# Optimization experiments

Hardware: AMD Instinct MI355X
Metric: run time of the kernel (lower is better)

## Reference

```python
import jax, jax.numpy as jnp
import numpy as np

T, B, E, H, P, D = 500, 1024, 26, 100, 80, 64  # frames, batch, embed, hidden, phonemes, dict_size


def gru_layer(xs, h0, Wih, Whh, bih, bhh):
    """PyTorch-convention GRU over time-major xs [T,B,in]; h0 [B,H]."""
    def step(h, x):
        gi = x @ Wih.T + bih          # [B,3H]
        gh = h @ Whh.T + bhh          # [B,3H]
        i_r, i_z, i_n = jnp.split(gi, 3, axis=-1)
        h_r, h_z, h_n = jnp.split(gh, 3, axis=-1)
        r = jax.nn.sigmoid(i_r + h_r)
        z = jax.nn.sigmoid(i_z + h_z)
        n = jnp.tanh(i_n + r * h_n)
        h_new = (1.0 - z) * n + z * h
        return h_new, h_new
    h_last, ys = jax.lax.scan(step, h0, xs)
    return ys, h_last


def _p(k, shape):
    return jax.random.normal(k, shape, dtype=jnp.float32) * 0.1


def setup_inputs() -> dict:
    key = jax.random.key(0)
    ks = jax.random.split(key, 20)
    inp = {
        "x": jax.random.normal(ks[0], (T, B, E), dtype=jnp.float32),
        "target": jax.random.randint(ks[1], (P, B, 1), 0, D).astype(jnp.int64),
        "emb": _p(ks[2], (D, E)),
        # encoder 2-layer GRU
        "enc_Wih0": _p(ks[3], (3 * H, E)), "enc_Whh0": _p(ks[4], (3 * H, H)),
        "enc_bih0": _p(ks[5], (3 * H,)),  "enc_bhh0": _p(ks[6], (3 * H,)),
        "enc_Wih1": _p(ks[7], (3 * H, H)), "enc_Whh1": _p(ks[8], (3 * H, H)),
        "enc_bih1": _p(ks[9], (3 * H,)),  "enc_bhh1": _p(ks[10], (3 * H,)),
        # decoder 2-layer GRU
        "dec_Wih0": _p(ks[11], (3 * H, E)), "dec_Whh0": _p(ks[12], (3 * H, H)),
        "dec_bih0": _p(ks[13], (3 * H,)),  "dec_bhh0": _p(ks[14], (3 * H,)),
        "dec_Wih1": _p(ks[15], (3 * H, H)), "dec_Whh1": _p(ks[16], (3 * H, H)),
        "dec_bih1": _p(ks[17], (3 * H,)),  "dec_bhh1": _p(ks[18], (3 * H,)),
        "lin_W": _p(ks[19], (D, H)),
        "lin_b": jnp.zeros((D,), dtype=jnp.float32),
    }
    return inp


def reference(x, target, emb,
              enc_Wih0, enc_Whh0, enc_bih0, enc_bhh0,
              enc_Wih1, enc_Whh1, enc_bih1, enc_bhh1,
              dec_Wih0, dec_Whh0, dec_bih0, dec_bhh0,
              dec_Wih1, dec_Whh1, dec_bih1, dec_bhh1,
              lin_W, lin_b):
    batch = x.shape[1]
    h0 = jnp.zeros((batch, H), dtype=x.dtype)
    # Encoder (dropout in eval mode = identity)
    e0, h_enc0 = gru_layer(x, h0, enc_Wih0, enc_Whh0, enc_bih0, enc_bhh0)
    e1, h_enc1 = gru_layer(e0, h0, enc_Wih1, enc_Whh1, enc_bih1, enc_bhh1)
    # Decoder with full teacher forcing: inputs are target[0..P-1]
    dec_in = emb[target[:, :, 0]]                       # [P,B,E]
    d0, _ = gru_layer(dec_in, h_enc0, dec_Wih0, dec_Whh0, dec_bih0, dec_bhh0)
    d1, _ = gru_layer(d0, h_enc1, dec_Wih1, dec_Whh1, dec_bih1, dec_bhh1)
    logits = d1 @ lin_W.T + lin_b                       # [P,B,D]
    softmax_cal = logits[:-1].reshape(-1, logits.shape[-1])  # [(P-1)*B, D]
    target_cal = target[1:].reshape(-1)                 # [(P-1)*B]
    asr_outputs = jnp.argmax(logits[:-1], axis=2)[:, :, None]  # [P-1,B,1]
    return softmax_cal, target_cal, asr_outputs
```

## Files before the change

### kernel.cpp

```cpp
#include <hip/hip_runtime.h>
#include <math.h>
#include <utility>

#define TB 1024
#define HH 100
#define GG 300

__device__ __forceinline__ float sigmoidf_(float x) {
    return 1.0f / (1.0f + expf(-x));
}
__device__ __forceinline__ float tanhf_(float x) {
    return tanhf(x);
}

template<size_t... Is>
__device__ __forceinline__ void ldN(std::index_sequence<Is...>,
                                    float* __restrict__ dst,
                                    const float* __restrict__ src) {
    ((dst[Is] = src[Is]), ...);
}
__device__ __forceinline__ float pin_val(float v) {
    asm volatile("" : "+v"(v));
    return v;
}
template<size_t... Is>
__device__ __forceinline__ void pinN(std::index_sequence<Is...>, float* w) {
    ((w[Is] = pin_val(w[Is])), ...);
}

template<int KK, int BT, int LD>
__device__ __forceinline__ void fma_step(const float* __restrict__ w,
                                         const float (*xs)[LD],
                                         float* __restrict__ acc) {
    #pragma unroll
    for (int b = 0; b < BT; ++b) {
        const float4 xv = *reinterpret_cast<const float4*>(&xs[b][KK]);
        acc[b] += w[KK]     * xv.x + w[KK + 1] * xv.y
                + w[KK + 2] * xv.z + w[KK + 3] * xv.w;
    }
}
template<int BT, int LD, size_t... Is>
__device__ __forceinline__ void gemv4(std::index_sequence<Is...>,
                                      const float* __restrict__ w,
                                      const float (*xs)[LD],
                                      float* __restrict__ acc) {
    (fma_step<(int)(Is * 4), BT, LD>(w, xs, acc), ...);
}

template<int GRP, int BT>
__device__ __forceinline__ void fma_lds_step(const float* __restrict__ wl,
                                             int row,
                                             const float (*hs)[HH],
                                             float* __restrict__ acc) {
    const float4 wv = *reinterpret_cast<const float4*>(wl + (GRP * GG + row) * 4);
    #pragma unroll
    for (int b = 0; b < BT; ++b) {
        const float4 hv = *reinterpret_cast<const float4*>(&hs[b][GRP * 4]);
        acc[b] += wv.x * hv.x + wv.y * hv.y + wv.z * hv.z + wv.w * hv.w;
    }
}
template<int BT, size_t... Is>
__device__ __forceinline__ void gemv_lds(std::index_sequence<Is...>,
                                         const float* __restrict__ wl, int row,
                                         const float (*hs)[HH],
                                         float* __restrict__ acc) {
    (fma_lds_step<(int)Is, BT>(wl, row, hs, acc), ...);
}

template<int K, bool EMB, bool WRITE_SEQ>
__global__ __launch_bounds__(640, 3)
void gru_kernel(const float* __restrict__ xin,
                const int*   __restrict__ tgt,
                const float* __restrict__ emb,
                const float* __restrict__ Wih,
                const float* __restrict__ Whh,
                const float* __restrict__ bih,
                const float* __restrict__ bhh,
                const float* __restrict__ h_init,
                float* __restrict__ seq_out,
                float* __restrict__ h_last,
                int T)
{
    constexpr int KP = (K + 3) & ~3;
    constexpr int BT = 2;
    constexpr int NT = 2;
    static_assert(KP % 4 == 0, "");

    const int tid  = threadIdx.x;
    const int team = tid / 320;
    const int tj   = tid % 320;
    const int bb0  = blockIdx.x * (BT * NT) + team * BT;
    const int g    = tj / 100;
    const int i    = tj % 100;

    __shared__ __align__(16) float whh_l[(HH / 4) * GG * 4];
    __shared__ __align__(16) float h_s[NT][BT][HH];
    __shared__ __align__(16) float x_s[NT][BT][KP];
    __shared__ float r_s[NT][BT][HH];
    __shared__ float z_s[NT][BT][HH];
    __shared__ float emb_s[EMB ? 64 : 1][EMB ? 28 : 4];
    __shared__ int   tgt_s[NT * BT];

    const int jj = (tj < GG) ? tj : 0;
    float wih[KP];
    ldN(std::make_index_sequence<K>{}, wih, Wih + (long)jj * K);
    #pragma unroll
    for (int k = K; k < KP; ++k) wih[k] = 0.f;
    float bi = bih[jj];
    float bh = bhh[jj];

    for (int idx = tid; idx < GG * HH; idx += 640) {
        int row = idx / HH, k = idx % HH;
        whh_l[((k >> 2) * GG + row) * 4 + (k & 3)] = Whh[row * HH + k];
    }

    for (int idx = tj; idx < BT * HH; idx += 320) {
        int b = idx / HH, k = idx % HH;
        h_s[team][b][k] = h_init ? h_init[(bb0 + b) * HH + k] : 0.f;
    }
    if constexpr (EMB) {
        for (int idx = tid; idx < 64 * 28; idx += 640) {
            int d = idx / 28, k = idx % 28;
            emb_s[d][k] = (k < 26) ? emb[d * 26 + k] : 0.f;
        }
        __syncthreads();
        for (int idx = tj; idx < BT * KP; idx += 320) {
            int b = idx / KP, k = idx % KP;
            int t0 = tgt[bb0 + b];
            x_s[team][b][k] = emb_s[t0][k];
        }
    } else {
        for (int idx = tj; idx < BT * KP; idx += 320) {
            int b = idx / KP, k = idx % KP;
            x_s[team][b][k] = (k < K) ? xin[(bb0 + b) * K + k] : 0.f;
        }
    }
    __syncthreads();

    for (int t = 0; t < T; ++t) {
        pinN(std::make_index_sequence<KP>{}, wih);
        bi = pin_val(bi);
        bh = pin_val(bh);

        const bool has_next = (t + 1 < T);

        float px = 0.f;
        int   ptg = 0;
        if constexpr (!EMB) {
            if (has_next && !(tj >= 200 && tj < 300)) {
                int stid = (tj < 200) ? tj : tj - 100;
                if (stid < BT * K)
                    px = xin[((t + 1) * TB + bb0 + stid / K) * K + stid % K];
            }
        } else {
            if (has_next && tj < BT) ptg = tgt[(t + 1) * TB + bb0 + tj];
        }

        float acc_i[BT], acc_h[BT];
        #pragma unroll
        for (int b = 0; b < BT; ++b) { acc_i[b] = bi; acc_h[b] = bh; }

        gemv4<BT, KP>(std::make_index_sequence<KP / 4>{}, wih, x_s[team], acc_i);
        gemv_lds<BT>(std::make_index_sequence<HH / 4>{}, whh_l, jj, h_s[team], acc_h);

        if (tj < 200) {
            #pragma unroll
            for (int b = 0; b < BT; ++b) {
                float v = sigmoidf_(acc_i[b] + acc_h[b]);
                if (g == 0) r_s[team][b][i] = v;
                else        z_s[team][b][i] = v;
            }
        }
        __syncthreads();

        if (tj >= 200 && tj < 300) {
            #pragma unroll
            for (int b = 0; b < BT; ++b) {
                float n  = tanhf_(acc_i[b] + r_s[team][b][i] * acc_h[b]);
                float z  = z_s[team][b][i];
                float hn = (1.f - z) * n + z * h_s[team][b][i];
                h_s[team][b][i] = hn;
                if (WRITE_SEQ)
                    seq_out[((long)t * TB + bb0 + b) * HH + i] = hn;
            }
        } else if constexpr (!EMB) {
            if (has_next) {
                int stid = (tj < 200) ? tj : tj - 100;
                if (stid < BT * K) x_s[team][stid / K][stid % K] = px;
            }
        }
        if constexpr (EMB) {
            if (has_next && tj < BT) tgt_s[team * BT + tj] = ptg;
            __syncthreads();
            if (has_next && tj < BT * KP) {
                int b = tj / KP, k = tj % KP;
                x_s[team][b][k] = emb_s[tgt_s[team * BT + b]][k];
            }
        }
        __syncthreads();
    }

    if (h_last != nullptr && tj >= 200 && tj < 300) {
        #pragma unroll
        for (int b = 0; b < BT; ++b)
            h_last[(bb0 + b) * HH + i] = h_s[team][b][i];
    }
}

__global__ __launch_bounds__(256)
void final_kernel(const float* __restrict__ d1,
                  const float* __restrict__ linW,
                  const float* __restrict__ linb,
                  const int*   __restrict__ tgt,
                  float* __restrict__ out0,
                  float* __restrict__ out1,
                  float* __restrict__ out2)
{
    __shared__ float WT[HH][64];
    __shared__ __align__(16) float row[4][HH];

    const int tid = threadIdx.x;
    for (int idx = tid; idx < 64 * HH; idx += 256) {
        int d = idx / HH, k = idx % HH;
        WT[k][d] = linW[idx];
    }
    const int s    = tid >> 6;
    const int d    = tid & 63;
    const int slot = blockIdx.x * 4 + s;
    const int p    = slot >> 10;
    const int b    = slot & 1023;
    const float* drow = &d1[(long)(p * TB + b) * HH];
    __syncthreads();
    if (d < 50) {
        float2 v = *reinterpret_cast<const float2*>(&drow[2 * d]);
        row[s][2 * d]     = v.x;
        row[s][2 * d + 1] = v.y;
    }
    __syncthreads();

    float acc = linb[d];
    #pragma unroll
    for (int k = 0; k < HH; ++k)
        acc += row[s][k] * WT[k][d];

    out0[(long)slot * 64 + d] = acc;

    float mv = acc;
    int   mi = d;
    #pragma unroll
    for (int off = 32; off >= 1; off >>= 1) {
        float ov = __shfl_xor(mv, off, 64);
        int   oi = __shfl_xor(mi, off, 64);
        if (ov > mv || (ov == mv && oi < mi)) { mv = ov; mi = oi; }
    }
    if (d == 0) out2[slot] = (float)mi;
    if (d == 1) out1[slot] = (float)tgt[(p + 1) * TB + b];
}

extern "C" void kernel_launch(void* const* d_in, const int* in_sizes, int n_in,
                              void* d_out, int out_size, void* d_ws, size_t ws_size,
                              hipStream_t stream)
{
    const float* x      = (const float*)d_in[0];
    const int*   target = (const int*)  d_in[1];
    const float* emb    = (const float*)d_in[2];
    const float* eWih0  = (const float*)d_in[3];
    const float* eWhh0  = (const float*)d_in[4];
    const float* ebih0  = (const float*)d_in[5];
    const float* ebhh0  = (const float*)d_in[6];
    const float* eWih1  = (const float*)d_in[7];
    const float* eWhh1  = (const float*)d_in[8];
    const float* ebih1  = (const float*)d_in[9];
    const float* ebhh1  = (const float*)d_in[10];
    const float* dWih0  = (const float*)d_in[11];
    const float* dWhh0  = (const float*)d_in[12];
    const float* dbih0  = (const float*)d_in[13];
    const float* dbhh0  = (const float*)d_in[14];
    const float* dWih1  = (const float*)d_in[15];
    const float* dWhh1  = (const float*)d_in[16];
    const float* dbih1  = (const float*)d_in[17];
    const float* dbhh1  = (const float*)d_in[18];
    const float* linW   = (const float*)d_in[19];
    const float* linb   = (const float*)d_in[20];

    float* ws     = (float*)d_ws;
    float* h_enc0 = ws;
    float* h_enc1 = ws + 102400;
    float* e0     = ws + 204800;
    float* d0     = ws + 204800;
    float* d1_    = ws + 204800 + 80 * 1024 * 100;

    dim3 grid(256), blk(640);
    gru_kernel<26,  false, true ><<<grid, blk, 0, stream>>>(
        x, nullptr, nullptr, eWih0, eWhh0, ebih0, ebhh0, nullptr, e0, h_enc0, 500);
    gru_kernel<100, false, false><<<grid, blk, 0, stream>>>(
        e0, nullptr, nullptr, eWih1, eWhh1, ebih1, ebhh1, nullptr, nullptr, h_enc1, 500);
    gru_kernel<26,  true,  true ><<<grid, blk, 0, stream>>>(
        nullptr, target, emb, dWih0, dWhh0, dbih0, dbhh0, h_enc0, d0, nullptr, 80);
    gru_kernel<100, false, true ><<<grid, blk, 0, stream>>>(
        d0, nullptr, nullptr, dWih1, dWhh1, dbih1, dbhh1, h_enc1, d1_, nullptr, 80);

    float* out0 = (float*)d_out;
    float* out1 = out0 + (long)79 * 1024 * 64;
    float* out2 = out1 + 79 * 1024;
    final_kernel<<<dim3(20224), dim3(256), 0, stream>>>(d1_, linW, linb, target,
                                                        out0, out1, out2);
}
```

Measured before the change: 3.578 ms.

## Keep GRU recurrent weights in registers and use one 320-thread team per block

Each thread now holds its row of the hidden-to-hidden weight matrix (100 floats) in registers instead of reading a transposed copy from LDS on every step. The two-team 640-thread block is replaced by a single 320-thread team that handles 4 batch rows, so the grid still covers the batch. This removes per-step LDS weight traffic and the LDS staging pass at kernel start. The cost is much higher register pressure: with the input weights also in registers (up to 100), a thread may need over 200 VGPRs, which limits occupancy and risks spills.

```diff
diff --git a/kernel.cpp b/kernel.cpp
--- a/kernel.cpp
+++ b/kernel.cpp
@@ -47,28 +47,8 @@
     (fma_step<(int)(Is * 4), BT, LD>(w, xs, acc), ...);
 }
 
-template<int GRP, int BT>
-__device__ __forceinline__ void fma_lds_step(const float* __restrict__ wl,
-                                             int row,
-                                             const float (*hs)[HH],
-                                             float* __restrict__ acc) {
-    const float4 wv = *reinterpret_cast<const float4*>(wl + (GRP * GG + row) * 4);
-    #pragma unroll
-    for (int b = 0; b < BT; ++b) {
-        const float4 hv = *reinterpret_cast<const float4*>(&hs[b][GRP * 4]);
-        acc[b] += wv.x * hv.x + wv.y * hv.y + wv.z * hv.z + wv.w * hv.w;
-    }
-}
-template<int BT, size_t... Is>
-__device__ __forceinline__ void gemv_lds(std::index_sequence<Is...>,
-                                         const float* __restrict__ wl, int row,
-                                         const float (*hs)[HH],
-                                         float* __restrict__ acc) {
-    (fma_lds_step<(int)Is, BT>(wl, row, hs, acc), ...);
-}
-
 template<int K, bool EMB, bool WRITE_SEQ>
-__global__ __launch_bounds__(640, 3)
+__global__ __launch_bounds__(320, 2)
 void gru_kernel(const float* __restrict__ xin,
                 const int*   __restrict__ tgt,
                 const float* __restrict__ emb,
@@ -82,44 +62,37 @@
                 int T)
 {
     constexpr int KP = (K + 3) & ~3;
-    constexpr int BT = 2;
-    constexpr int NT = 2;
+    constexpr int BT = 4;
     static_assert(KP % 4 == 0, "");
 
-    const int tid  = threadIdx.x;
-    const int team = tid / 320;
-    const int tj   = tid % 320;
-    const int bb0  = blockIdx.x * (BT * NT) + team * BT;
-    const int g    = tj / 100;
-    const int i    = tj % 100;
-
-    __shared__ __align__(16) float whh_l[(HH / 4) * GG * 4];
-    __shared__ __align__(16) float h_s[NT][BT][HH];
-    __shared__ __align__(16) float x_s[NT][BT][KP];
-    __shared__ float r_s[NT][BT][HH];
-    __shared__ float z_s[NT][BT][HH];
+    const int tj  = threadIdx.x;
+    const int bb0 = blockIdx.x * BT;
+    const int g   = tj / 100;
+    const int i   = tj % 100;
+
+    __shared__ __align__(16) float h_s[BT][HH];
+    __shared__ __align__(16) float x_s[BT][KP];
+    __shared__ float r_s[BT][HH];
+    __shared__ float z_s[BT][HH];
     __shared__ float emb_s[EMB ? 64 : 1][EMB ? 28 : 4];
-    __shared__ int   tgt_s[NT * BT];
+    __shared__ int   tgt_s[BT];
 
     const int jj = (tj < GG) ? tj : 0;
     float wih[KP];
     ldN(std::make_index_sequence<K>{}, wih, Wih + (long)jj * K);
     #pragma unroll
     for (int k = K; k < KP; ++k) wih[k] = 0.f;
+    float whr[HH];
+    ldN(std::make_index_sequence<HH>{}, whr, Whh + (long)jj * HH);
     float bi = bih[jj];
     float bh = bhh[jj];
 
-    for (int idx = tid; idx < GG * HH; idx += 640) {
-        int row = idx / HH, k = idx % HH;
-        whh_l[((k >> 2) * GG + row) * 4 + (k & 3)] = Whh[row * HH + k];
-    }
-
     for (int idx = tj; idx < BT * HH; idx += 320) {
         int b = idx / HH, k = idx % HH;
-        h_s[team][b][k] = h_init ? h_init[(bb0 + b) * HH + k] : 0.f;
+        h_s[b][k] = h_init ? h_init[(bb0 + b) * HH + k] : 0.f;
     }
     if constexpr (EMB) {
-        for (int idx = tid; idx < 64 * 28; idx += 640) {
+        for (int idx = tj; idx < 64 * 28; idx += 320) {
             int d = idx / 28, k = idx % 28;
             emb_s[d][k] = (k < 26) ? emb[d * 26 + k] : 0.f;
         }
@@ -127,30 +100,35 @@
         for (int idx = tj; idx < BT * KP; idx += 320) {
             int b = idx / KP, k = idx % KP;
             int t0 = tgt[bb0 + b];
-            x_s[team][b][k] = emb_s[t0][k];
+            x_s[b][k] = emb_s[t0][k];
         }
     } else {
         for (int idx = tj; idx < BT * KP; idx += 320) {
             int b = idx / KP, k = idx % KP;
-            x_s[team][b][k] = (k < K) ? xin[(bb0 + b) * K + k] : 0.f;
+            x_s[b][k] = (k < K) ? xin[(bb0 + b) * K + k] : 0.f;
         }
     }
     __syncthreads();
 
     for (int t = 0; t < T; ++t) {
         pinN(std::make_index_sequence<KP>{}, wih);
+        pinN(std::make_index_sequence<HH>{}, whr);
         bi = pin_val(bi);
         bh = pin_val(bh);
 
         const bool has_next = (t + 1 < T);
 
-        float px = 0.f;
+        float px0 = 0.f, px1 = 0.f;
         int   ptg = 0;
         if constexpr (!EMB) {
-            if (has_next && !(tj >= 200 && tj < 300)) {
-                int stid = (tj < 200) ? tj : tj - 100;
-                if (stid < BT * K)
-                    px = xin[((t + 1) * TB + bb0 + stid / K) * K + stid % K];
+            if (has_next) {
+                if (tj < BT * K)
+                    px0 = xin[((t + 1) * TB + bb0 + tj / K) * K + tj % K];
+                if constexpr (BT * K > 320) {
+                    if (tj + 320 < BT * K)
+                        px1 = xin[((t + 1) * TB + bb0 + (tj + 320) / K) * K
+                                  + (tj + 320) % K];
+                }
             }
         } else {
             if (has_next && tj < BT) ptg = tgt[(t + 1) * TB + bb0 + tj];
@@ -160,15 +138,15 @@
         #pragma unroll
         for (int b = 0; b < BT; ++b) { acc_i[b] = bi; acc_h[b] = bh; }
 
-        gemv4<BT, KP>(std::make_index_sequence<KP / 4>{}, wih, x_s[team], acc_i);
-        gemv_lds<BT>(std::make_index_sequence<HH / 4>{}, whh_l, jj, h_s[team], acc_h);
+        gemv4<BT, KP>(std::make_index_sequence<KP / 4>{}, wih, x_s, acc_i);
+        gemv4<BT, HH>(std::make_index_sequence<HH / 4>{}, whr, h_s, acc_h);
 
         if (tj < 200) {
             #pragma unroll
             for (int b = 0; b < BT; ++b) {
                 float v = sigmoidf_(acc_i[b] + acc_h[b]);
-                if (g == 0) r_s[team][b][i] = v;
-                else        z_s[team][b][i] = v;
+                if (g == 0) r_s[b][i] = v;
+                else        z_s[b][i] = v;
             }
         }
         __syncthreads();
@@ -176,25 +154,28 @@
         if (tj >= 200 && tj < 300) {
             #pragma unroll
             for (int b = 0; b < BT; ++b) {
-                float n  = tanhf_(acc_i[b] + r_s[team][b][i] * acc_h[b]);
-                float z  = z_s[team][b][i];
-                float hn = (1.f - z) * n + z * h_s[team][b][i];
-                h_s[team][b][i] = hn;
+                float n  = tanhf_(acc_i[b] + r_s[b][i] * acc_h[b]);
+                float z  = z_s[b][i];
+                float hn = (1.f - z) * n + z * h_s[b][i];
+                h_s[b][i] = hn;
                 if (WRITE_SEQ)
                     seq_out[((long)t * TB + bb0 + b) * HH + i] = hn;
             }
-        } else if constexpr (!EMB) {
+        }
+        if constexpr (!EMB) {
             if (has_next) {
-                int stid = (tj < 200) ? tj : tj - 100;
-                if (stid < BT * K) x_s[team][stid / K][stid % K] = px;
-            }
-        }
-        if constexpr (EMB) {
-            if (has_next && tj < BT) tgt_s[team * BT + tj] = ptg;
+                if (tj < BT * K) x_s[tj / K][tj % K] = px0;
+                if constexpr (BT * K > 320) {
+                    if (tj + 320 < BT * K)
+                        x_s[(tj + 320) / K][(tj + 320) % K] = px1;
+                }
+            }
+        } else {
+            if (has_next && tj < BT) tgt_s[tj] = ptg;
             __syncthreads();
             if (has_next && tj < BT * KP) {
                 int b = tj / KP, k = tj % KP;
-                x_s[team][b][k] = emb_s[tgt_s[team * BT + b]][k];
+                x_s[b][k] = emb_s[tgt_s[b]][k];
             }
         }
         __syncthreads();
@@ -203,7 +184,7 @@
     if (h_last != nullptr && tj >= 200 && tj < 300) {
         #pragma unroll
         for (int b = 0; b < BT; ++b)
-            h_last[(bb0 + b) * HH + i] = h_s[team][b][i];
+            h_last[(bb0 + b) * HH + i] = h_s[b][i];
     }
 }
 
@@ -290,7 +271,7 @@
     float* d0     = ws + 204800;
     float* d1_    = ws + 204800 + 80 * 1024 * 100;
 
-    dim3 grid(256), blk(640);
+    dim3 grid(256), blk(320);
     gru_kernel<26,  false, true ><<<grid, blk, 0, stream>>>(
         x, nullptr, nullptr, eWih0, eWhh0, ebih0, ebhh0, nullptr, e0, h_enc0, 500);
     gru_kernel<100, false, false><<<grid, blk, 0, stream>>>(
```

Result: slower. 4.800 ms (+34.2%).

## Split GRU kernel: register-resident Whh for small-input layers, LDS Whh for others

Applied to the files above, without the earlier changes.

Adds a 320-thread kernel for the layers with 26-wide input, where each thread keeps its full Whh row (100 floats) in registers instead of reading a transposed copy from LDS. One block now covers 2 batch rows, so the grid grows to 512 blocks. The layers with 100-wide input keep the LDS-based Whh path in a simplified kernel with the embedding branch removed. The aim is to remove LDS traffic from the recurrent GEMV in the first layers, at the cost of heavy register pressure (about 130 pinned floats per thread) and possible spills under the forced 3 waves per EU.

```diff
diff --git a/kernel.cpp b/kernel.cpp
--- a/kernel.cpp
+++ b/kernel.cpp
@@ -68,18 +68,147 @@
 }
 
 template<int K, bool EMB, bool WRITE_SEQ>
-__global__ __launch_bounds__(640, 3)
-void gru_kernel(const float* __restrict__ xin,
-                const int*   __restrict__ tgt,
-                const float* __restrict__ emb,
-                const float* __restrict__ Wih,
-                const float* __restrict__ Whh,
-                const float* __restrict__ bih,
-                const float* __restrict__ bhh,
-                const float* __restrict__ h_init,
-                float* __restrict__ seq_out,
-                float* __restrict__ h_last,
-                int T)
+__global__ __launch_bounds__(320)
+__attribute__((amdgpu_waves_per_eu(3, 3)))
+void gru_small(const float* __restrict__ xin,
+               const int*   __restrict__ tgt,
+               const float* __restrict__ emb,
+               const float* __restrict__ Wih,
+               const float* __restrict__ Whh,
+               const float* __restrict__ bih,
+               const float* __restrict__ bhh,
+               const float* __restrict__ h_init,
+               float* __restrict__ seq_out,
+               float* __restrict__ h_last,
+               int T)
+{
+    constexpr int KP = (K + 3) & ~3;
+    constexpr int BT = 2;
+    static_assert(KP % 4 == 0, "");
+    static_assert(BT * K <= 320, "");
+
+    const int tj  = threadIdx.x;
+    const int bb0 = blockIdx.x * BT;
+    const int g   = tj / 100;
+    const int i   = tj % 100;
+
+    __shared__ __align__(16) float h_s[BT][HH];
+    __shared__ __align__(16) float x_s[BT][KP];
+    __shared__ float r_s[BT][HH];
+    __shared__ float z_s[BT][HH];
+    __shared__ float emb_s[EMB ? 64 : 1][EMB ? 28 : 4];
+    __shared__ int   tgt_s[BT];
+
+    const int jj = (tj < GG) ? tj : 0;
+    float wih[KP];
+    ldN(std::make_index_sequence<K>{}, wih, Wih + (long)jj * K);
+    #pragma unroll
+    for (int k = K; k < KP; ++k) wih[k] = 0.f;
+    float whr[HH];
+    ldN(std::make_index_sequence<HH>{}, whr, Whh + (long)jj * HH);
+    float bi = bih[jj];
+    float bh = bhh[jj];
+
+    for (int idx = tj; idx < BT * HH; idx += 320) {
+        int b = idx / HH, k = idx % HH;
+        h_s[b][k] = h_init ? h_init[(bb0 + b) * HH + k] : 0.f;
+    }
+    if constexpr (EMB) {
+        for (int idx = tj; idx < 64 * 28; idx += 320) {
+            int d = idx / 28, k = idx % 28;
+            emb_s[d][k] = (k < 26) ? emb[d * 26 + k] : 0.f;
+        }
+        __syncthreads();
+        for (int idx = tj; idx < BT * KP; idx += 320) {
+            int b = idx / KP, k = idx % KP;
+            int t0 = tgt[bb0 + b];
+            x_s[b][k] = emb_s[t0][k];
+        }
+    } else {
+        for (int idx = tj; idx < BT * KP; idx += 320) {
+            int b = idx / KP, k = idx % KP;
+            x_s[b][k] = (k < K) ? xin[(bb0 + b) * K + k] : 0.f;
+        }
+    }
+    __syncthreads();
+
+    for (int t = 0; t < T; ++t) {
+        pinN(std::make_index_sequence<KP>{}, wih);
+        pinN(std::make_index_sequence<HH>{}, whr);
+        bi = pin_val(bi);
+        bh = pin_val(bh);
+
+        const bool has_next = (t + 1 < T);
+
+        float px0 = 0.f;
+        int   ptg = 0;
+        if constexpr (!EMB) {
+            if (has_next && tj < BT * K)
+                px0 = xin[((t + 1) * TB + bb0 + tj / K) * K + tj % K];
+        } else {
+            if (has_next && tj < BT) ptg = tgt[(t + 1) * TB + bb0 + tj];
+        }
+
+        float acc_i[BT], acc_h[BT];
+        #pragma unroll
+        for (int b = 0; b < BT; ++b) { acc_i[b] = bi; acc_h[b] = bh; }
+
+        gemv4<BT, KP>(std::make_index_sequence<KP / 4>{}, wih, x_s, acc_i);
+        gemv4<BT, HH>(std::make_index_sequence<HH / 4>{}, whr, h_s, acc_h);
+
+        if (tj < 200) {
+            #pragma unroll
+            for (int b = 0; b < BT; ++b) {
+                float v = sigmoidf_(acc_i[b] + acc_h[b]);
+                if (g == 0) r_s[b][i] = v;
+                else        z_s[b][i] = v;
+            }
+        }
+        __syncthreads();
+
+        if (tj >= 200 && tj < 300) {
+            #pragma unroll
+            for (int b = 0; b < BT; ++b) {
+                float n  = tanhf_(acc_i[b] + r_s[b][i] * acc_h[b]);
+                float z  = z_s[b][i];
+                float hn = (1.f - z) * n + z * h_s[b][i];
+                h_s[b][i] = hn;
+                if (WRITE_SEQ)
+                    seq_out[((long)t * TB + bb0 + b) * HH + i] = hn;
+            }
+        }
+        if constexpr (!EMB) {
+            if (has_next && tj < BT * K) x_s[tj / K][tj % K] = px0;
+        } else {
+            if (has_next && tj < BT) tgt_s[tj] = ptg;
+            __syncthreads();
+            if (has_next && tj < BT * KP) {
+                int b = tj / KP, k = tj % KP;
+                x_s[b][k] = emb_s[tgt_s[b]][k];
+            }
+        }
+        __syncthreads();
+    }
+
+    if (h_last != nullptr && tj >= 200 && tj < 300) {
+        #pragma unroll
+        for (int b = 0; b < BT; ++b)
+            h_last[(bb0 + b) * HH + i] = h_s[b][i];
+    }
+}
+
+template<int K, bool WRITE_SEQ>
+__global__ __launch_bounds__(640)
+__attribute__((amdgpu_waves_per_eu(3, 3)))
+void gru_big(const float* __restrict__ xin,
+             const float* __restrict__ Wih,
+             const float* __restrict__ Whh,
+             const float* __restrict__ bih,
+             const float* __restrict__ bhh,
+             const float* __restrict__ h_init,
+             float* __restrict__ seq_out,
+             float* __restrict__ h_last,
+             int T)
 {
     constexpr int KP = (K + 3) & ~3;
     constexpr int BT = 2;
@@ -98,8 +227,6 @@
     __shared__ __align__(16) float x_s[NT][BT][KP];
     __shared__ float r_s[NT][BT][HH];
     __shared__ float z_s[NT][BT][HH];
-    __shared__ float emb_s[EMB ? 64 : 1][EMB ? 28 : 4];
-    __shared__ int   tgt_s[NT * BT];
 
     const int jj = (tj < GG) ? tj : 0;
     float wih[KP];
@@ -118,22 +245,9 @@
         int b = idx / HH, k = idx % HH;
         h_s[team][b][k] = h_init ? h_init[(bb0 + b) * HH + k] : 0.f;
     }
-    if constexpr (EMB) {
-        for (int idx = tid; idx < 64 * 28; idx += 640) {
-            int d = idx / 28, k = idx % 28;
-            emb_s[d][k] = (k < 26) ? emb[d * 26 + k] : 0.f;
-        }
-        __syncthreads();
-        for (int idx = tj; idx < BT * KP; idx += 320) {
-            int b = idx / KP, k = idx % KP;
-            int t0 = tgt[bb0 + b];
-            x_s[team][b][k] = emb_s[t0][k];
-        }
-    } else {
-        for (int idx = tj; idx < BT * KP; idx += 320) {
-            int b = idx / KP, k = idx % KP;
-            x_s[team][b][k] = (k < K) ? xin[(bb0 + b) * K + k] : 0.f;
-        }
+    for (int idx = tj; idx < BT * KP; idx += 320) {
+        int b = idx / KP, k = idx % KP;
+        x_s[team][b][k] = (k < K) ? xin[(bb0 + b) * K + k] : 0.f;
     }
     __syncthreads();
 
@@ -145,15 +259,10 @@
         const bool has_next = (t + 1 < T);
 
         float px = 0.f;
-        int   ptg = 0;
-        if constexpr (!EMB) {
-            if (has_next && !(tj >= 200 && tj < 300)) {
-                int stid = (tj < 200) ? tj : tj - 100;
-                if (stid < BT * K)
-                    px = xin[((t + 1) * TB + bb0 + stid / K) * K + stid % K];
-            }
-        } else {
-            if (has_next && tj < BT) ptg = tgt[(t + 1) * TB + bb0 + tj];
+        if (has_next && !(tj >= 200 && tj < 300)) {
+            int stid = (tj < 200) ? tj : tj - 100;
+            if (stid < BT * K)
+                px = xin[((t + 1) * TB + bb0 + stid / K) * K + stid % K];
         }
 
         float acc_i[BT], acc_h[BT];
@@ -183,18 +292,10 @@
                 if (WRITE_SEQ)
                     seq_out[((long)t * TB + bb0 + b) * HH + i] = hn;
             }
-        } else if constexpr (!EMB) {
+        } else {
             if (has_next) {
                 int stid = (tj < 200) ? tj : tj - 100;
                 if (stid < BT * K) x_s[team][stid / K][stid % K] = px;
-            }
-        }
-        if constexpr (EMB) {
-            if (has_next && tj < BT) tgt_s[team * BT + tj] = ptg;
-            __syncthreads();
-            if (has_next && tj < BT * KP) {
-                int b = tj / KP, k = tj % KP;
-                x_s[team][b][k] = emb_s[tgt_s[team * BT + b]][k];
             }
         }
         __syncthreads();
@@ -290,15 +391,14 @@
     float* d0     = ws + 204800;
     float* d1_    = ws + 204800 + 80 * 1024 * 100;
 
-    dim3 grid(256), blk(640);
-    gru_kernel<26,  false, true ><<<grid, blk, 0, stream>>>(
+    gru_small<26, false, true ><<<dim3(512), dim3(320), 0, stream>>>(
         x, nullptr, nullptr, eWih0, eWhh0, ebih0, ebhh0, nullptr, e0, h_enc0, 500);
-    gru_kernel<100, false, false><<<grid, blk, 0, stream>>>(
-        e0, nullptr, nullptr, eWih1, eWhh1, ebih1, ebhh1, nullptr, nullptr, h_enc1, 500);
-    gru_kernel<26,  true,  true ><<<grid, blk, 0, stream>>>(
+    gru_big<100, false><<<dim3(256), dim3(640), 0, stream>>>(
+        e0, eWih1, eWhh1, ebih1, ebhh1, nullptr, nullptr, h_enc1, 500);
+    gru_small<26, true,  true ><<<dim3(512), dim3(320), 0, stream>>>(
         nullptr, target, emb, dWih0, dWhh0, dbih0, dbhh0, h_enc0, d0, nullptr, 80);
-    gru_kernel<100, false, true ><<<grid, blk, 0, stream>>>(
-        d0, nullptr, nullptr, dWih1, dWhh1, dbih1, dbhh1, h_enc1, d1_, nullptr, 80);
+    gru_big<100, true ><<<dim3(256), dim3(640), 0, stream>>>(
+        d0, dWih1, dWhh1, dbih1, dbhh1, h_enc1, d1_, nullptr, 80);
 
     float* out0 = (float*)d_out;
     float* out1 = out0 + (long)79 * 1024 * 64;
```

After: 4.421 ms. +23.6%, slower.

## Split GRU kernel into small-input and big-input variants with register-resident Whh slice

Applied to the files above, without the earlier changes.

The K=26 GRU layers get a dedicated kernel that processes one batch row per team, launches twice as many blocks, and keeps the first 40 columns of Whh in registers while the remaining 60 stay in LDS. This shrinks per-block LDS and targets higher occupancy (waves_per_eu 5). The embedding lookup now reads global memory directly instead of going through an LDS table and an extra barrier. The K=100 layers move to a separate kernel with the asm register pinning removed and launch bounds relaxed, which could raise register spills or change scheduling.

```diff
diff --git a/kernel.cpp b/kernel.cpp
--- a/kernel.cpp
+++ b/kernel.cpp
@@ -18,14 +18,6 @@
                                     float* __restrict__ dst,
                                     const float* __restrict__ src) {
     ((dst[Is] = src[Is]), ...);
-}
-__device__ __forceinline__ float pin_val(float v) {
-    asm volatile("" : "+v"(v));
-    return v;
-}
-template<size_t... Is>
-__device__ __forceinline__ void pinN(std::index_sequence<Is...>, float* w) {
-    ((w[Is] = pin_val(w[Is])), ...);
 }
 
 template<int KK, int BT, int LD>
@@ -47,44 +39,149 @@
     (fma_step<(int)(Is * 4), BT, LD>(w, xs, acc), ...);
 }
 
-template<int GRP, int BT>
+template<int GRP, int OFF, int BT>
 __device__ __forceinline__ void fma_lds_step(const float* __restrict__ wl,
                                              int row,
                                              const float (*hs)[HH],
                                              float* __restrict__ acc) {
-    const float4 wv = *reinterpret_cast<const float4*>(wl + (GRP * GG + row) * 4);
+    const float4 wv =
+        *reinterpret_cast<const float4*>(wl + ((GRP - OFF) * GG + row) * 4);
     #pragma unroll
     for (int b = 0; b < BT; ++b) {
         const float4 hv = *reinterpret_cast<const float4*>(&hs[b][GRP * 4]);
         acc[b] += wv.x * hv.x + wv.y * hv.y + wv.z * hv.z + wv.w * hv.w;
     }
 }
-template<int BT, size_t... Is>
+template<int OFF, int BT, size_t... Is>
 __device__ __forceinline__ void gemv_lds(std::index_sequence<Is...>,
                                          const float* __restrict__ wl, int row,
                                          const float (*hs)[HH],
                                          float* __restrict__ acc) {
-    (fma_lds_step<(int)Is, BT>(wl, row, hs, acc), ...);
-}
-
-template<int K, bool EMB, bool WRITE_SEQ>
-__global__ __launch_bounds__(640, 3)
-void gru_kernel(const float* __restrict__ xin,
-                const int*   __restrict__ tgt,
-                const float* __restrict__ emb,
-                const float* __restrict__ Wih,
-                const float* __restrict__ Whh,
-                const float* __restrict__ bih,
-                const float* __restrict__ bhh,
-                const float* __restrict__ h_init,
-                float* __restrict__ seq_out,
-                float* __restrict__ h_last,
-                int T)
+    (fma_lds_step<(int)Is + OFF, OFF, BT>(wl, row, hs, acc), ...);
+}
+
+template<bool EMB, bool WRITE_SEQ>
+__global__ __launch_bounds__(640)
+__attribute__((amdgpu_waves_per_eu(5, 5)))
+void gru_small(const float* __restrict__ xin,
+               const int*   __restrict__ tgt,
+               const float* __restrict__ emb,
+               const float* __restrict__ Wih,
+               const float* __restrict__ Whh,
+               const float* __restrict__ bih,
+               const float* __restrict__ bhh,
+               const float* __restrict__ h_init,
+               float* __restrict__ seq_out,
+               float* __restrict__ h_last,
+               int T)
 {
-    constexpr int KP = (K + 3) & ~3;
+    constexpr int K    = 26;
+    constexpr int KP   = 28;
+    constexpr int KREG = 40;
+    constexpr int KLDS = HH - KREG;
+
+    const int tid  = threadIdx.x;
+    const int team = tid / 320;
+    const int tj   = tid % 320;
+    const int bb   = blockIdx.x * 2 + team;
+    const int g    = tj / 100;
+    const int i    = tj % 100;
+
+    __shared__ __align__(16) float whh_l[(KLDS / 4) * GG * 4];
+    __shared__ __align__(16) float h_s[2][1][HH];
+    __shared__ __align__(16) float x_s[2][1][KP];
+    __shared__ float r_s[2][HH];
+    __shared__ float z_s[2][HH];
+
+    const int jj = (tj < GG) ? tj : 0;
+    float wih[KP];
+    ldN(std::make_index_sequence<K>{}, wih, Wih + (long)jj * K);
+    #pragma unroll
+    for (int k = K; k < KP; ++k) wih[k] = 0.f;
+    float whr[KREG];
+    ldN(std::make_index_sequence<KREG>{}, whr, Whh + (long)jj * HH);
+    float bi = bih[jj];
+    float bh = bhh[jj];
+
+    for (int idx = tid; idx < GG * KLDS; idx += 640) {
+        int row = idx / KLDS, kk = idx % KLDS;
+        whh_l[((kk >> 2) * GG + row) * 4 + (kk & 3)] = Whh[row * HH + KREG + kk];
+    }
+
+    for (int idx = tj; idx < HH; idx += 320)
+        h_s[team][0][idx] = h_init ? h_init[bb * HH + idx] : 0.f;
+    if (tj < KP) {
+        if constexpr (EMB) {
+            int t0 = tgt[bb];
+            x_s[team][0][tj] = (tj < K) ? emb[t0 * K + tj] : 0.f;
+        } else {
+            x_s[team][0][tj] = (tj < K) ? xin[bb * K + tj] : 0.f;
+        }
+    }
+    __syncthreads();
+
+    for (int t = 0; t < T; ++t) {
+        const bool has_next = (t + 1 < T);
+
+        float px = 0.f;
+        if (has_next && tj < KP) {
+            if constexpr (EMB) {
+                int ptg = tgt[(t + 1) * TB + bb];
+                px = (tj < K) ? emb[ptg * K + tj] : 0.f;
+            } else {
+                if (tj < K) px = xin[((t + 1) * TB + bb) * K + tj];
+            }
+        }
+
+        float acc_i[1], acc_h[1];
+        acc_i[0] = bi;
+        acc_h[0] = bh;
+
+        gemv4<1, KP>(std::make_index_sequence<KP / 4>{}, wih, x_s[team], acc_i);
+        gemv4<1, HH>(std::make_index_sequence<KREG / 4>{}, whr, h_s[team], acc_h);
+        gemv_lds<KREG / 4, 1>(std::make_index_sequence<KLDS / 4>{},
+                              whh_l, jj, h_s[team], acc_h);
+
+        if (tj < 200) {
+            float v = sigmoidf_(acc_i[0] + acc_h[0]);
+            if (g == 0) r_s[team][i] = v;
+            else        z_s[team][i] = v;
+        }
+        __syncthreads();
+
+        if (tj >= 200 && tj < 300) {
+            float n  = tanhf_(acc_i[0] + r_s[team][i] * acc_h[0]);
+            float z  = z_s[team][i];
+            float hn = (1.f - z) * n + z * h_s[team][0][i];
+            h_s[team][0][i] = hn;
+            if (WRITE_SEQ)
+                seq_out[((long)t * TB + bb) * HH + i] = hn;
+        } else if (has_next && tj < KP) {
+            x_s[team][0][tj] = px;
+        }
+        __syncthreads();
+    }
+
+    if (h_last != nullptr && tj >= 200 && tj < 300)
+        h_last[bb * HH + i] = h_s[team][0][i];
+}
+
+template<bool WRITE_SEQ>
+__global__ __launch_bounds__(640)
+void gru_big(const float* __restrict__ xin,
+             const float* __restrict__ Wih,
+             const float* __restrict__ Whh,
+             const float* __restrict__ bih,
+             const float* __restrict__ bhh,
+             const float* __restrict__ h_init,
+             float* __restrict__ seq_out,
+             float* __restrict__ h_last,
+             int T)
+{
+    constexpr int K  = 100;
+    constexpr int KP = 100;
     constexpr int BT = 2;
     constexpr int NT = 2;
-    static_assert(KP % 4 == 0, "");
 
     const int tid  = threadIdx.x;
     const int team = tid / 320;
@@ -98,14 +195,10 @@
     __shared__ __align__(16) float x_s[NT][BT][KP];
     __shared__ float r_s[NT][BT][HH];
     __shared__ float z_s[NT][BT][HH];
-    __shared__ float emb_s[EMB ? 64 : 1][EMB ? 28 : 4];
-    __shared__ int   tgt_s[NT * BT];
 
     const int jj = (tj < GG) ? tj : 0;
     float wih[KP];
     ldN(std::make_index_sequence<K>{}, wih, Wih + (long)jj * K);
-    #pragma unroll
-    for (int k = K; k < KP; ++k) wih[k] = 0.f;
     float bi = bih[jj];
     float bh = bhh[jj];
 
@@ -118,42 +211,20 @@
         int b = idx / HH, k = idx % HH;
         h_s[team][b][k] = h_init ? h_init[(bb0 + b) * HH + k] : 0.f;
     }
-    if constexpr (EMB) {
-        for (int idx = tid; idx < 64 * 28; idx += 640) {
-            int d = idx / 28, k = idx % 28;
-            emb_s[d][k] = (k < 26) ? emb[d * 26 + k] : 0.f;
-        }
-        __syncthreads();
-        for (int idx = tj; idx < BT * KP; idx += 320) {
-            int b = idx / KP, k = idx % KP;
-            int t0 = tgt[bb0 + b];
-            x_s[team][b][k] = emb_s[t0][k];
-        }
-    } else {
-        for (int idx = tj; idx < BT * KP; idx += 320) {
-            int b = idx / KP, k = idx % KP;
-            x_s[team][b][k] = (k < K) ? xin[(bb0 + b) * K + k] : 0.f;
-        }
+    for (int idx = tj; idx < BT * KP; idx += 320) {
+        int b = idx / KP, k = idx % KP;
+        x_s[team][b][k] = xin[(bb0 + b) * K + k];
     }
     __syncthreads();
 
     for (int t = 0; t < T; ++t) {
-        pinN(std::make_index_sequence<KP>{}, wih);
-        bi = pin_val(bi);
-        bh = pin_val(bh);
-
         const bool has_next = (t + 1 < T);
 
         float px = 0.f;
-        int   ptg = 0;
-        if constexpr (!EMB) {
-            if (has_next && !(tj >= 200 && tj < 300)) {
-                int stid = (tj < 200) ? tj : tj - 100;
-                if (stid < BT * K)
-                    px = xin[((t + 1) * TB + bb0 + stid / K) * K + stid % K];
-            }
-        } else {
-            if (has_next && tj < BT) ptg = tgt[(t + 1) * TB + bb0 + tj];
+        if (has_next && !(tj >= 200 && tj < 300)) {
+            int stid = (tj < 200) ? tj : tj - 100;
+            if (stid < BT * K)
+                px = xin[((t + 1) * TB + bb0 + stid / K) * K + stid % K];
         }
 
         float acc_i[BT], acc_h[BT];
@@ -161,7 +232,8 @@
         for (int b = 0; b < BT; ++b) { acc_i[b] = bi; acc_h[b] = bh; }
 
         gemv4<BT, KP>(std::make_index_sequence<KP / 4>{}, wih, x_s[team], acc_i);
-        gemv_lds<BT>(std::make_index_sequence<HH / 4>{}, whh_l, jj, h_s[team], acc_h);
+        gemv_lds<0, BT>(std::make_index_sequence<HH / 4>{},
+                        whh_l, jj, h_s[team], acc_h);
 
         if (tj < 200) {
             #pragma unroll
@@ -183,18 +255,10 @@
                 if (WRITE_SEQ)
                     seq_out[((long)t * TB + bb0 + b) * HH + i] = hn;
             }
-        } else if constexpr (!EMB) {
+        } else {
             if (has_next) {
                 int stid = (tj < 200) ? tj : tj - 100;
                 if (stid < BT * K) x_s[team][stid / K][stid % K] = px;
-            }
-        }
-        if constexpr (EMB) {
-            if (has_next && tj < BT) tgt_s[team * BT + tj] = ptg;
-            __syncthreads();
-            if (has_next && tj < BT * KP) {
-                int b = tj / KP, k = tj % KP;
-                x_s[team][b][k] = emb_s[tgt_s[team * BT + b]][k];
             }
         }
         __syncthreads();
@@ -290,15 +354,14 @@
     float* d0     = ws + 204800;
     float* d1_    = ws + 204800 + 80 * 1024 * 100;
 
-    dim3 grid(256), blk(640);
-    gru_kernel<26,  false, true ><<<grid, blk, 0, stream>>>(
+    gru_small<false, true ><<<dim3(512), dim3(640), 0, stream>>>(
         x, nullptr, nullptr, eWih0, eWhh0, ebih0, ebhh0, nullptr, e0, h_enc0, 500);
-    gru_kernel<100, false, false><<<grid, blk, 0, stream>>>(
-        e0, nullptr, nullptr, eWih1, eWhh1, ebih1, ebhh1, nullptr, nullptr, h_enc1, 500);
-    gru_kernel<26,  true,  true ><<<grid, blk, 0, stream>>>(
+    gru_big<false><<<dim3(256), dim3(640), 0, stream>>>(
+        e0, eWih1, eWhh1, ebih1, ebhh1, nullptr, nullptr, h_enc1, 500);
+    gru_small<true,  true ><<<dim3(512), dim3(640), 0, stream>>>(
         nullptr, target, emb, dWih0, dWhh0, dbih0, dbhh0, h_enc0, d0, nullptr, 80);
-    gru_kernel<100, false, true ><<<grid, blk, 0, stream>>>(
-        d0, nullptr, nullptr, dWih1, dWhh1, dbih1, dbhh1, h_enc1, d1_, nullptr, 80);
+    gru_big<true ><<<dim3(256), dim3(640), 0, stream>>>(
+        d0, dWih1, dWhh1, dbih1, dbhh1, h_enc1, d1_, nullptr, 80);
 
     float* out0 = (float*)d_out;
     float* out1 = out0 + (long)79 * 1024 * 64;
```

Result: slower. 3.973 ms (+11.1%).
